# Performance work log

Measured on AMD Instinct MI355X. Metric: run time of the kernel, lower is better.

The kernel has to match this reference:

```python
import jax, jax.numpy as jnp
import numpy as np
from jax.scipy.special import i0

IM_SIZE = (256, 256)
GRID_SIZE = (512, 512)
NUMPOINTS = 6
OS = GRID_SIZE[0] / IM_SIZE[0]
# Beatty et al. optimal Kaiser-Bessel shape parameter
BETA = float(np.pi * np.sqrt((NUMPOINTS / OS) ** 2 * (OS - 0.5) ** 2 - 0.8))


def _apod_1d(N, G):
    # 1/FT(kb kernel) scaling coefficients (de-apodization), static numpy
    x = np.arange(N) - N / 2.0
    arg = np.pi * NUMPOINTS * x / G
    t = BETA ** 2 - arg ** 2  # > 0 for this config
    ph = np.sinh(np.sqrt(t)) / np.sqrt(t)
    return (1.0 / ph).astype(np.float32)


def _kb(u):
    # Kaiser-Bessel interpolation kernel, support |u| <= NUMPOINTS/2
    x = 2.0 * u / NUMPOINTS
    t = 1.0 - x * x
    inside = t > 0
    t = jnp.where(inside, t, 0.0)
    return jnp.where(inside, i0(BETA * jnp.sqrt(t)), 0.0)


def setup_inputs():
    key = jax.random.key(0)
    k1, k2, k3 = jax.random.split(key, 3)
    B, M = 8, 131072
    image = jax.random.normal(k1, (B,) + IM_SIZE, dtype=jnp.float32)
    ktraj = (jax.random.uniform(k2, (B, 2, M), dtype=jnp.float32) * 2.0 - 1.0) * jnp.pi
    dcf = jax.random.uniform(k3, (B, M), dtype=jnp.float32)
    return {"image": image, "ktraj": ktraj, "dcf": dcf}


def _nufft(image, ktraj, dcf):
    B = image.shape[0]
    N1, N2 = IM_SIZE
    G1, G2 = GRID_SIZE
    J = NUMPOINTS
    # 1) de-apodization (scaling coefficients), separable per-dim
    a1 = jnp.asarray(_apod_1d(N1, G1))
    a2 = jnp.asarray(_apod_1d(N2, G2))
    img = image.astype(jnp.complex64) * (a1[:, None] * a2[None, :])
    # 2) centered zero-pad to oversampled grid, FFT with DC at bin 0
    p1, p2 = (G1 - N1) // 2, (G2 - N2) // 2
    grid = jnp.zeros((B, G1, G2), dtype=jnp.complex64).at[:, p1:p1 + N1, p2:p2 + N2].set(img)
    kgrid = jnp.fft.fft2(jnp.fft.ifftshift(grid, axes=(1, 2)))
    # 3) KB interpolation (gather) at non-uniform points
    tm1 = ktraj[:, 0] * (G1 / (2.0 * jnp.pi))  # (B,M) in grid units
    tm2 = ktraj[:, 1] * (G2 / (2.0 * jnp.pi))
    offs = jnp.arange(J, dtype=jnp.float32) - (J // 2 - 1)  # [-2..3]
    g1 = jnp.floor(tm1)[..., None] + offs  # (B,M,J) neighbor coords
    g2 = jnp.floor(tm2)[..., None] + offs
    w1 = _kb(tm1[..., None] - g1)
    w2 = _kb(tm2[..., None] - g2)
    i1 = jnp.mod(g1.astype(jnp.int32), G1)
    i2 = jnp.mod(g2.astype(jnp.int32), G2)
    lin = (i1[..., :, None] * G2 + i2[..., None, :]).reshape(B, -1)  # (B, M*J*J)
    vals = jnp.take_along_axis(kgrid.reshape(B, -1), lin, axis=1).reshape(B, -1, J, J)
    w = (w1[..., :, None] * w2[..., None, :]).astype(jnp.complex64)
    kdata = jnp.sum(vals * w, axis=(-1, -2))  # (B,M) complex
    kdata = kdata * dcf
    return jnp.stack([kdata.real, kdata.imag], axis=0)  # (2,B,M) float32


def reference(image, ktraj, dcf):
    return _nufft(image, ktraj, dcf)
```

## Files before the change

kernel.cpp:

```cpp
#include <hip/hip_runtime.h>
#include <math.h>

#define GSZ 512
#define NSZ 256
#define NBATCH 8
#define MPTS 131072
#define PI_F 3.14159265358979f
#define BETA_F 13.8551004f
#define BETA2_F (BETA_F * BETA_F)
#define RSQ2 0.70710678f
#define PADIDX(i) ((i) + ((i) >> 3))

typedef float f32x4 __attribute__((ext_vector_type(4)));


__device__ __forceinline__ float apod(int i) {
    float x = (float)(i - 128);
    float arg = PI_F * 6.0f * x * (1.0f / 512.0f);
    float t = BETA2_F - arg * arg;
    float st = sqrtf(t);
    return 2.0f * st * __expf(-st);
}

__device__ __forceinline__ float kbw(float u) {
    float t = 1.0f - u * u * (1.0f / 9.0f);
    float x = BETA_F * sqrtf(fmaxf(t, 0.0f));
    float xc = fmaxf(x, 0.35f);
    float R = __builtin_amdgcn_rsqf(xc);
    float R2 = R * R;
    float q = R * (0.39894228f + R2 * (0.04986779f + R2 * 0.02804702f));
    float w = __expf(xc) * q;
    return (t > 0.0f) ? w : 0.0f;
}

template<int CTRL>
__device__ __forceinline__ float qdpp(float v) {
    int r = __builtin_amdgcn_mov_dpp(__float_as_int(v), CTRL, 0xF, 0xF, true);
    return __int_as_float(r);
}

__device__ __forceinline__ float2 cadd(float2 a, float2 b){ return make_float2(a.x+b.x, a.y+b.y); }
__device__ __forceinline__ float2 csub(float2 a, float2 b){ return make_float2(a.x-b.x, a.y-b.y); }
__device__ __forceinline__ float2 cmul(float2 a, float2 b){ return make_float2(a.x*b.x-a.y*b.y, a.x*b.y+a.y*b.x); }
__device__ __forceinline__ float2 mul_negi(float2 a){ return make_float2(a.y, -a.x); }
__device__ __forceinline__ float2 mul_posi(float2 a){ return make_float2(-a.y, a.x); }
__device__ __forceinline__ float2 mul_w81(float2 a){ return make_float2(RSQ2*(a.x+a.y), RSQ2*(a.y-a.x)); }
__device__ __forceinline__ float2 mul_w83(float2 a){ return make_float2(RSQ2*(a.y-a.x), -RSQ2*(a.x+a.y)); }

__device__ __forceinline__ void dft8_combine(float2 E0, float2 E1, float2 E2, float2 E3,
                                             float2 O0, float2 O1, float2 O2, float2 O3,
                                             float2* y) {
    float2 c1 = mul_w81(O1), c2 = mul_negi(O2), c3 = mul_w83(O3);
    y[0] = cadd(E0, O0); y[4] = csub(E0, O0);
    y[1] = cadd(E1, c1); y[5] = csub(E1, c1);
    y[2] = cadd(E2, c2); y[6] = csub(E2, c2);
    y[3] = cadd(E3, c3); y[7] = csub(E3, c3);
}

__device__ __forceinline__ void dft8(const float2* x, float2* y) {
    float2 a0=x[0], a1=x[2], a2=x[4], a3=x[6];
    float2 b0=x[1], b1=x[3], b2=x[5], b3=x[7];
    float2 ta0=cadd(a0,a2), ta1=csub(a0,a2), ta2=cadd(a1,a3), ta3=csub(a1,a3);
    float2 E0=cadd(ta0,ta2), E2=csub(ta0,ta2);
    float2 E1=cadd(ta1, mul_negi(ta3)), E3=cadd(ta1, mul_posi(ta3));
    float2 tb0=cadd(b0,b2), tb1=csub(b0,b2), tb2=cadd(b1,b3), tb3=csub(b1,b3);
    float2 O0=cadd(tb0,tb2), O2=csub(tb0,tb2);
    float2 O1=cadd(tb1, mul_negi(tb3)), O3=cadd(tb1, mul_posi(tb3));
    dft8_combine(E0,E1,E2,E3,O0,O1,O2,O3,y);
}

__device__ __forceinline__ void dft8_pruned(float2 x0, float2 x1, float2 x6, float2 x7, float2* y) {
    float2 E0 = cadd(x0, x6), E2 = csub(x0, x6);
    float2 E1 = cadd(x0, mul_posi(x6)), E3 = cadd(x0, mul_negi(x6));
    float2 O0 = cadd(x1, x7), O2 = csub(x1, x7);
    float2 O1 = cadd(x1, mul_posi(x7)), O3 = cadd(x1, mul_negi(x7));
    dft8_combine(E0,E1,E2,E3,O0,O1,O2,O3,y);
}

template<int S>
__device__ __forceinline__ void twiddle8(int t, float2* y) {
    if (S < 2) {
        int j = (S == 0) ? t : (t >> 3);
        const float scale = (S == 0) ? (-2.0f*PI_F/512.0f) : (-2.0f*PI_F/64.0f);
        float theta = scale * (float)j;
        float sn, cs;
        __sincosf(theta, &sn, &cs);
        float2 w = make_float2(cs, sn), wq = w;
        y[1] = cmul(y[1], wq);
        #pragma unroll
        for (int q = 2; q < 8; ++q) { wq = cmul(wq, w); y[q] = cmul(y[q], wq); }
    }
}


__device__ __forceinline__ float2 pswap(float2 v) {
    return make_float2(qdpp<0xB1>(v.x), qdpp<0xB1>(v.y));
}

__device__ __forceinline__ void dft8_half(const float2* v, float2* EO) {
    float2 t0 = cadd(v[0], v[2]), t1 = csub(v[0], v[2]);
    float2 t2 = cadd(v[1], v[3]), t3 = csub(v[1], v[3]);
    EO[0] = cadd(t0, t2); EO[2] = csub(t0, t2);
    EO[1] = cadd(t1, mul_negi(t3)); EO[3] = cadd(t1, mul_posi(t3));
}

__device__ __forceinline__ void dft8p_half(float2 u0, float2 u1, float2* EO) {
    EO[0] = cadd(u0, u1); EO[2] = csub(u0, u1);
    EO[1] = cadd(u0, mul_posi(u1)); EO[3] = cadd(u0, mul_negi(u1));
}

__device__ __forceinline__ void combine_half(int h, const float2* V, float2* y) {
    float2 P0 = pswap(V[0]), P1 = pswap(V[1]), P2 = pswap(V[2]), P3 = pswap(V[3]);
    float2 E0 = h ? P0 : V[0], O0 = h ? V[0] : P0;
    float2 E1 = h ? P1 : V[1], O1 = h ? V[1] : P1;
    float2 E2 = h ? P2 : V[2], O2 = h ? V[2] : P2;
    float2 E3 = h ? P3 : V[3], O3 = h ? V[3] : P3;
    float2 c1 = mul_w81(O1), c2 = mul_negi(O2), c3 = mul_w83(O3);
    float s = h ? -1.0f : 1.0f;
    y[0] = make_float2(fmaf(s, O0.x, E0.x), fmaf(s, O0.y, E0.y));
    y[1] = make_float2(fmaf(s, c1.x, E1.x), fmaf(s, c1.y, E1.y));
    y[2] = make_float2(fmaf(s, c2.x, E2.x), fmaf(s, c2.y, E2.y));
    y[3] = make_float2(fmaf(s, c3.x, E3.x), fmaf(s, c3.y, E3.y));
}

__device__ __forceinline__ void twiddle4h(int jidx, float scale, int h, float2* y) {
    float theta = scale * (float)jidx;
    float sn, cs;
    __sincosf(theta, &sn, &cs);
    float2 w = make_float2(cs, sn);
    float2 w2 = cmul(w, w);
    float2 w4 = cmul(w2, w2);
    float2 m = h ? w4 : make_float2(1.0f, 0.0f);
    y[0] = cmul(y[0], m);
    float2 wq = cmul(m, w); y[1] = cmul(y[1], wq);
    wq = cmul(wq, w);       y[2] = cmul(y[2], wq);
    wq = cmul(wq, w);       y[3] = cmul(y[3], wq);
}

__global__ __launch_bounds__(256) void pass1_rowfft(const float* __restrict__ image,
                                                    float2* __restrict__ T,
                                                    const float* __restrict__ ktraj,
                                                    const float* __restrict__ dcf,
                                                    int* __restrict__ cursors,
                                                    float4* __restrict__ sortedpt) {
    __shared__ float4 smemBuf[2176];
    int tid = threadIdx.x;
    int blk = blockIdx.x;

    if (blk >= 512) {
        int u = blk - 512;
        int bs = u >> 6, seg = u & 63;
        const float SCALE = (float)GSZ / (2.0f * PI_F);
        const float* kt1 = ktraj + (size_t)(bs * 2) * MPTS;
        const float* kt2 = kt1 + MPTS;
        const float* dcfb = dcf + ((size_t)bs << 17);
        int* cur = cursors + (bs << 7);
        float4* sp = sortedpt + ((size_t)bs << 18);

        float4* pts = smemBuf;
        int* hist = (int*)(smemBuf + 2048);
        int* lofs = hist + 128;
        int* gbase = hist + 256;
        int* lcur = hist + 384;

        if (tid < 128) hist[tid] = 0;
        __syncthreads();

        float t1v[8], t2v[8], dv[8];
        #pragma unroll
        for (int k = 0; k < 8; ++k) {
            int m = (seg << 11) + (k << 8) + tid;
            t1v[k] = kt1[m] * SCALE;
            t2v[k] = kt2[m] * SCALE;
            dv[k]  = dcfb[m];
            int key = (((int)floorf(t2v[k])) & 511) >> 2;
            atomicAdd(&hist[key], 1);
        }
        __syncthreads();

        if (tid == 0) {
            int s = 0;
            #pragma unroll 8
            for (int i = 0; i < 128; ++i) { lofs[i] = s; s += hist[i]; }
        }
        if (tid < 128) { gbase[tid] = atomicAdd(cur + tid, hist[tid]); lcur[tid] = 0; }
        __syncthreads();

        #pragma unroll
        for (int k = 0; k < 8; ++k) {
            int m = (seg << 11) + (k << 8) + tid;
            int key = (((int)floorf(t2v[k])) & 511) >> 2;
            int loc = atomicAdd(&lcur[key], 1);
            pts[lofs[key] + loc] =
                make_float4(t1v[k], t2v[k], dv[k], __int_as_float((key << 17) | m));
        }
        __syncthreads();

        #pragma unroll
        for (int k = 0; k < 8; ++k) {
            int s = (k << 8) + tid;
            float4 p = pts[s];
            int w = __float_as_int(p.w);
            int key = w >> 17;
            int m = w & 0x1FFFF;
            int gpos = gbase[key] + (s - lofs[key]);
            if (gpos < 2048)
                sp[((size_t)key << 11) + gpos] =
                    make_float4(p.x, p.y, p.z, __int_as_float(m));
        }
        return;
    }

    float2 (*sm)[2][578] = reinterpret_cast<float2(*)[2][578]>(smemBuf);
    int r = tid >> 7;
    int tt = tid & 127;
    int h = tt & 1;
    int b = tt >> 1;
    int p = blk & 3;
    int g = blk >> 2;
    int rp = (g << 1) + r;
    int y = (rp < 128) ? rp : (rp + 256);
    int iy = (y < 128) ? (y + 128) : (y - 384);
    float ay = apod(iy);
    const float* irow0 = image + ((size_t)((2 * p)     * NSZ + iy)) * NSZ;
    const float* irow1 = image + ((size_t)((2 * p + 1) * NSZ + iy)) * NSZ;

    float2 y4[4];
    {
        int iA = h ? (b + 192) : (b + 128);
        int iB = h ? (b + 64)  : b;
        float wA = ay * apod(iA), wB = ay * apod(iB);
        float2 u0 = make_float2(irow0[iA] * wA, irow1[iA] * wA);
        float2 u1 = make_float2(irow0[iB] * wB, irow1[iB] * wB);
        float2 EO[4];
        dft8p_half(u0, u1, EO);
        combine_half(h, EO, y4);
        twiddle4h(b, -2.0f * PI_F / 512.0f, h, y4);
    }
    float2* A  = sm[0][r];
    float2* Bf = sm[1][r];
    #pragma unroll
    for (int qq = 0; qq < 4; ++qq) A[PADIDX((b << 3) + (h << 2) + qq)] = y4[qq];
    __syncthreads();
    {
        float2 v[4];
        #pragma unroll
        for (int i = 0; i < 4; ++i) v[i] = A[PADIDX(b + (((i << 1) + h) << 6))];
        float2 EO[4];
        dft8_half(v, EO);
        combine_half(h, EO, y4);
        twiddle4h(b >> 3, -2.0f * PI_F / 64.0f, h, y4);
        int base = (b & 7) + ((b >> 3) << 6);
        #pragma unroll
        for (int qq = 0; qq < 4; ++qq) Bf[PADIDX(base + (((h << 2) + qq) << 3))] = y4[qq];
    }
    __syncthreads();
    {
        float2 v[4];
        #pragma unroll
        for (int i = 0; i < 4; ++i) v[i] = Bf[PADIDX(b + (((i << 1) + h) << 6))];
        float2 EO[4];
        dft8_half(v, EO);
        combine_half(h, EO, y4);
        float2* Trow = T + (((size_t)(p << 8) + rp) << 9);
        #pragma unroll
        for (int qq = 0; qq < 4; ++qq) Trow[b + (((h << 2) + qq) << 6)] = y4[qq];
    }
}

__global__ __launch_bounds__(256) void pass2_colfft(const float2* __restrict__ T,
                                                    float2* __restrict__ kgridT) {
    __shared__ float2 B[8][578];
    int tid = threadIdx.x;
    int blk = blockIdx.x;
    int p = blk & 3;
    int g = blk >> 2;
    const float2* Tb = T + ((size_t)p << 17);
    float2* Kb0 = kgridT + ((size_t)(2 * p) << 18);
    float2* Kb1 = Kb0 + ((size_t)1 << 18);

    #define COLG(c) ((g > 0) ? (((c) < 4) ? ((g << 2) + (c)) : (505 - (g << 2) + (c))) \
                             : (((c) < 4) ? (c) : (((c) == 7) ? 256 : (505 + (c)))))

    {
        int c = tid & 7, r0 = tid >> 3;
        int colg = COLG(c);
        #pragma unroll
        for (int k = 0; k < 8; ++k) {
            int rr = r0 + (k << 5);
            B[c][PADIDX(rr)] = Tb[((size_t)rr << 9) + colg];
        }
    }
    __syncthreads();
    int t = tid & 63;
    int c0 = tid >> 6;
    float2* Ba = B[c0];
    float2* Bb = B[c0 + 4];
    float2 ya[8], yb[8];
    {
        float2 a0 = Ba[PADIDX(t)],       a1 = Ba[PADIDX(t + 64)];
        float2 a6 = Ba[PADIDX(t + 128)], a7 = Ba[PADIDX(t + 192)];
        float2 b0 = Bb[PADIDX(t)],       b1 = Bb[PADIDX(t + 64)];
        float2 b6 = Bb[PADIDX(t + 128)], b7 = Bb[PADIDX(t + 192)];
        dft8_pruned(a0, a1, a6, a7, ya); twiddle8<0>(t, ya);
        dft8_pruned(b0, b1, b6, b7, yb); twiddle8<0>(t, yb);
    }
    __syncthreads();
    #pragma unroll
    for (int q = 0; q < 8; ++q) {
        Ba[PADIDX((t << 3) + q)] = ya[q];
        Bb[PADIDX((t << 3) + q)] = yb[q];
    }
    __syncthreads();
    {
        float2 xa[8], xb[8];
        #pragma unroll
        for (int pp = 0; pp < 8; ++pp) { xa[pp] = Ba[PADIDX(t + (pp << 6))]; xb[pp] = Bb[PADIDX(t + (pp << 6))]; }
        dft8(xa, ya); twiddle8<1>(t, ya);
        dft8(xb, yb); twiddle8<1>(t, yb);
    }
    __syncthreads();
    {
        int j = t >> 3, k = t & 7, base = k + (j << 6);
        #pragma unroll
        for (int q = 0; q < 8; ++q) {
            Ba[PADIDX(base + (q << 3))] = ya[q];
            Bb[PADIDX(base + (q << 3))] = yb[q];
        }
    }
    __syncthreads();
    {
        float2 xa[8], xb[8];
        #pragma unroll
        for (int pp = 0; pp < 8; ++pp) { xa[pp] = Ba[PADIDX(t + (pp << 6))]; xb[pp] = Bb[PADIDX(t + (pp << 6))]; }
        dft8(xa, ya);
        dft8(xb, yb);
    }
    __syncthreads();
    #pragma unroll
    for (int q = 0; q < 8; ++q) {
        Ba[PADIDX(t + (q << 6))] = ya[q];
        Bb[PADIDX(t + (q << 6))] = yb[q];
    }
    __syncthreads();
    {
        int c = tid & 7, r0 = tid >> 3;
        int colg = COLG(c);
        int mc = 7 - c;
        if (g == 0) { if (c == 0) mc = 0; else if (c == 7) mc = 7; }
        #pragma unroll
        for (int k = 0; k < 16; ++k) {
            int rr = r0 + (k << 5);
            int mr = (512 - rr) & 511;
            float2 Z = B[c][PADIDX(rr)];
            float2 M = B[mc][PADIDX(mr)];
            float2 K0 = make_float2(0.5f * (Z.x + M.x), 0.5f * (Z.y - M.y));
            float2 K1 = make_float2(0.5f * (Z.y + M.y), 0.5f * (M.x - Z.x));
            size_t off = ((size_t)colg << 9) + rr;
            Kb0[off] = K0;
            Kb1[off] = K1;
        }
    }
    #undef COLG
}

__global__ __launch_bounds__(256) void interp_kb(const float2* __restrict__ kgridT,
                                                 const int* __restrict__ cursors,
                                                 const float4* __restrict__ sortedpt,
                                                 float* __restrict__ out) {
    __shared__ float lds[9 * 1028];
    int tid = threadIdx.x;
    int blk = blockIdx.x;
    int b = blk & 7;
    int band = blk >> 3;
    int j = tid & 3;
    int q = tid >> 2;
    int j2 = j << 1;
    float fjm2 = (float)(j - 2), fjp2 = (float)(j + 2);

    int cnt = cursors[(b << 7) + band];
    cnt = (cnt > 2048) ? 2048 : cnt;
    if (cnt == 0) return;

    const float2* Kb = kgridT + ((size_t)b << 18);
    #pragma unroll
    for (int r = 0; r < 9; ++r) {
        int gc = ((band << 2) - 2 + r) & 511;
        const float4* src = (const float4*)(Kb + ((size_t)gc << 9));
        *(float4*)(lds + r * 1028 + (tid << 2)) = src[tid];
    }
    __syncthreads();

    const float4* sp = sortedpt + ((size_t)b << 18) + ((size_t)band << 11);
    float* out_re = out + ((size_t)b << 17);
    float* out_im = out_re + (size_t)NBATCH * MPTS;

    int iters = (cnt + 63) >> 6;
    for (int it = 0; it < iters; ++it) {
        int pidx = (it << 6) + q;
        bool valid = pidx < cnt;
        float4 pt = sp[valid ? pidx : 0];
        float tm1 = pt.x, tm2 = pt.y, dd = pt.z;
        int m = __float_as_int(pt.w);

        float f1 = floorf(tm1), f2 = floorf(tm2);
        int if1 = (int)f1, if2 = (int)f2;
        int e1 = (if1 - 2) & ~1;
        int rpair = (e1 + j2) & 511;
        int csoff = (if2 & 511) - (band << 2);

        float u1 = tm1 - (float)(e1 + j2);
        float wra = kbw(u1);
        float wrb = kbw(u1 - 1.0f);
        float fr2 = tm2 - f2;
        float wA = kbw(fr2 - fjm2);
        float wB = kbw(fr2 - fjp2);
        float w0_ = qdpp<0x00>(wA);
        float w1_ = qdpp<0x55>(wA);
        float w2_ = qdpp<0xAA>(wA);
        float w3_ = qdpp<0xFF>(wA);
        float w4_ = qdpp<0x00>(wB);
        float w5_ = qdpp<0x55>(wB);

        const float* lp = lds + (rpair << 1) + csoff * 1028;
        f32x4 v0 = *(const f32x4*)(lp + 0 * 1028);
        f32x4 v1 = *(const f32x4*)(lp + 1 * 1028);
        f32x4 v2 = *(const f32x4*)(lp + 2 * 1028);
        f32x4 v3 = *(const f32x4*)(lp + 3 * 1028);
        f32x4 v4 = *(const f32x4*)(lp + 4 * 1028);
        f32x4 v5 = *(const f32x4*)(lp + 5 * 1028);

        float c0re = w0_ * v0.x, c0im = w0_ * v0.y;
        float c1re = w0_ * v0.z, c1im = w0_ * v0.w;
        c0re = fmaf(w1_, v1.x, c0re); c0im = fmaf(w1_, v1.y, c0im);
        c1re = fmaf(w1_, v1.z, c1re); c1im = fmaf(w1_, v1.w, c1im);
        c0re = fmaf(w2_, v2.x, c0re); c0im = fmaf(w2_, v2.y, c0im);
        c1re = fmaf(w2_, v2.z, c1re); c1im = fmaf(w2_, v2.w, c1im);
        c0re = fmaf(w3_, v3.x, c0re); c0im = fmaf(w3_, v3.y, c0im);
        c1re = fmaf(w3_, v3.z, c1re); c1im = fmaf(w3_, v3.w, c1im);
        c0re = fmaf(w4_, v4.x, c0re); c0im = fmaf(w4_, v4.y, c0im);
        c1re = fmaf(w4_, v4.z, c1re); c1im = fmaf(w4_, v4.w, c1im);
        c0re = fmaf(w5_, v5.x, c0re); c0im = fmaf(w5_, v5.y, c0im);
        c1re = fmaf(w5_, v5.z, c1re); c1im = fmaf(w5_, v5.w, c1im);
        float p_re = fmaf(wra, c0re, wrb * c1re);
        float p_im = fmaf(wra, c0im, wrb * c1im);
        p_re += qdpp<0xB1>(p_re); p_re += qdpp<0x4E>(p_re);
        p_im += qdpp<0xB1>(p_im); p_im += qdpp<0x4E>(p_im);

        if (valid) {
            if (j == 0) out_re[m] = p_re * dd;
            else if (j == 1) out_im[m] = p_im * dd;
        }
    }
}


extern "C" void kernel_launch(void* const* d_in, const int* in_sizes, int n_in,
                              void* d_out, int out_size, void* d_ws, size_t ws_size,
                              hipStream_t stream) {
    const float* image = (const float*)d_in[0];
    const float* ktraj = (const float*)d_in[1];
    const float* dcf   = (const float*)d_in[2];
    float* out = (float*)d_out;

    float2* T        = (float2*)d_ws;
    float2* kgridT   = T + (size_t)4 * 256 * GSZ;
    int*    cursors  = (int*)((char*)d_ws + 20971520);
    float4* sortedpt = (float4*)((char*)d_ws + 20975616);

    hipMemsetAsync(cursors, 0, 1024 * sizeof(int), stream);
    pass1_rowfft<<<1024, 256, 0, stream>>>(image, T, ktraj, dcf, cursors, sortedpt);
    pass2_colfft<<<256, 256, 0, stream>>>(T, kgridT);
    interp_kb<<<1024, 256, 0, stream>>>(kgridT, cursors, sortedpt, out);
}
```

Baseline: 120.9 us.

## Split column FFT across 1024 threads with half-radix work and skip zero-weight LDS loads

The column FFT kernel now launches 1024 threads per block instead of 256. Each thread pair shares one radix-8 butterfly through the half-DFT and DPP combine helpers already used in the row pass, so each thread holds 4 values instead of 16. The old full dft8 helpers are deleted. In the interpolation kernel, the six LDS vector loads are now guarded so they are skipped when both row weights are zero. The changes aim to raise parallelism and cut register pressure in the column pass, at the cost of more threads per block and cross-lane shuffles. The guard adds a branch that may cause divergence.

```diff
diff --git a/kernel.cpp b/kernel.cpp
--- a/kernel.cpp
+++ b/kernel.cpp
@@ -46,51 +46,6 @@
 __device__ __forceinline__ float2 mul_posi(float2 a){ return make_float2(-a.y, a.x); }
 __device__ __forceinline__ float2 mul_w81(float2 a){ return make_float2(RSQ2*(a.x+a.y), RSQ2*(a.y-a.x)); }
 __device__ __forceinline__ float2 mul_w83(float2 a){ return make_float2(RSQ2*(a.y-a.x), -RSQ2*(a.x+a.y)); }
-
-__device__ __forceinline__ void dft8_combine(float2 E0, float2 E1, float2 E2, float2 E3,
-                                             float2 O0, float2 O1, float2 O2, float2 O3,
-                                             float2* y) {
-    float2 c1 = mul_w81(O1), c2 = mul_negi(O2), c3 = mul_w83(O3);
-    y[0] = cadd(E0, O0); y[4] = csub(E0, O0);
-    y[1] = cadd(E1, c1); y[5] = csub(E1, c1);
-    y[2] = cadd(E2, c2); y[6] = csub(E2, c2);
-    y[3] = cadd(E3, c3); y[7] = csub(E3, c3);
-}
-
-__device__ __forceinline__ void dft8(const float2* x, float2* y) {
-    float2 a0=x[0], a1=x[2], a2=x[4], a3=x[6];
-    float2 b0=x[1], b1=x[3], b2=x[5], b3=x[7];
-    float2 ta0=cadd(a0,a2), ta1=csub(a0,a2), ta2=cadd(a1,a3), ta3=csub(a1,a3);
-    float2 E0=cadd(ta0,ta2), E2=csub(ta0,ta2);
-    float2 E1=cadd(ta1, mul_negi(ta3)), E3=cadd(ta1, mul_posi(ta3));
-    float2 tb0=cadd(b0,b2), tb1=csub(b0,b2), tb2=cadd(b1,b3), tb3=csub(b1,b3);
-    float2 O0=cadd(tb0,tb2), O2=csub(tb0,tb2);
-    float2 O1=cadd(tb1, mul_negi(tb3)), O3=cadd(tb1, mul_posi(tb3));
-    dft8_combine(E0,E1,E2,E3,O0,O1,O2,O3,y);
-}
-
-__device__ __forceinline__ void dft8_pruned(float2 x0, float2 x1, float2 x6, float2 x7, float2* y) {
-    float2 E0 = cadd(x0, x6), E2 = csub(x0, x6);
-    float2 E1 = cadd(x0, mul_posi(x6)), E3 = cadd(x0, mul_negi(x6));
-    float2 O0 = cadd(x1, x7), O2 = csub(x1, x7);
-    float2 O1 = cadd(x1, mul_posi(x7)), O3 = cadd(x1, mul_negi(x7));
-    dft8_combine(E0,E1,E2,E3,O0,O1,O2,O3,y);
-}
-
-template<int S>
-__device__ __forceinline__ void twiddle8(int t, float2* y) {
-    if (S < 2) {
-        int j = (S == 0) ? t : (t >> 3);
-        const float scale = (S == 0) ? (-2.0f*PI_F/512.0f) : (-2.0f*PI_F/64.0f);
-        float theta = scale * (float)j;
-        float sn, cs;
-        __sincosf(theta, &sn, &cs);
-        float2 w = make_float2(cs, sn), wq = w;
-        y[1] = cmul(y[1], wq);
-        #pragma unroll
-        for (int q = 2; q < 8; ++q) { wq = cmul(wq, w); y[q] = cmul(y[q], wq); }
-    }
-}
 
 
 __device__ __forceinline__ float2 pswap(float2 v) {
@@ -268,8 +223,8 @@
     }
 }
 
-__global__ __launch_bounds__(256) void pass2_colfft(const float2* __restrict__ T,
-                                                    float2* __restrict__ kgridT) {
+__global__ __launch_bounds__(1024) void pass2_colfft(const float2* __restrict__ T,
+                                                     float2* __restrict__ kgridT) {
     __shared__ float2 B[8][578];
     int tid = threadIdx.x;
     int blk = blockIdx.x;
@@ -286,62 +241,59 @@
         int c = tid & 7, r0 = tid >> 3;
         int colg = COLG(c);
         #pragma unroll
-        for (int k = 0; k < 8; ++k) {
-            int rr = r0 + (k << 5);
+        for (int k = 0; k < 2; ++k) {
+            int rr = r0 + (k << 7);
             B[c][PADIDX(rr)] = Tb[((size_t)rr << 9) + colg];
         }
     }
     __syncthreads();
-    int t = tid & 63;
-    int c0 = tid >> 6;
-    float2* Ba = B[c0];
-    float2* Bb = B[c0 + 4];
-    float2 ya[8], yb[8];
-    {
-        float2 a0 = Ba[PADIDX(t)],       a1 = Ba[PADIDX(t + 64)];
-        float2 a6 = Ba[PADIDX(t + 128)], a7 = Ba[PADIDX(t + 192)];
-        float2 b0 = Bb[PADIDX(t)],       b1 = Bb[PADIDX(t + 64)];
-        float2 b6 = Bb[PADIDX(t + 128)], b7 = Bb[PADIDX(t + 192)];
-        dft8_pruned(a0, a1, a6, a7, ya); twiddle8<0>(t, ya);
-        dft8_pruned(b0, b1, b6, b7, yb); twiddle8<0>(t, yb);
+
+    int s = tid >> 7;
+    int tt = tid & 127;
+    int h = tt & 1;
+    int b = tt >> 1;
+    float2* Bs = B[s];
+    float2 y4[4];
+
+    {
+        float2 u0 = Bs[PADIDX(b + (h << 6))];
+        float2 u1 = Bs[PADIDX(b + 128 + (h << 6))];
+        float2 EO[4];
+        dft8p_half(u0, u1, EO);
+        combine_half(h, EO, y4);
+        twiddle4h(b, -2.0f * PI_F / 512.0f, h, y4);
     }
     __syncthreads();
     #pragma unroll
-    for (int q = 0; q < 8; ++q) {
-        Ba[PADIDX((t << 3) + q)] = ya[q];
-        Bb[PADIDX((t << 3) + q)] = yb[q];
-    }
-    __syncthreads();
-    {
-        float2 xa[8], xb[8];
-        #pragma unroll
-        for (int pp = 0; pp < 8; ++pp) { xa[pp] = Ba[PADIDX(t + (pp << 6))]; xb[pp] = Bb[PADIDX(t + (pp << 6))]; }
-        dft8(xa, ya); twiddle8<1>(t, ya);
-        dft8(xb, yb); twiddle8<1>(t, yb);
-    }
-    __syncthreads();
-    {
-        int j = t >> 3, k = t & 7, base = k + (j << 6);
-        #pragma unroll
-        for (int q = 0; q < 8; ++q) {
-            Ba[PADIDX(base + (q << 3))] = ya[q];
-            Bb[PADIDX(base + (q << 3))] = yb[q];
-        }
-    }
-    __syncthreads();
-    {
-        float2 xa[8], xb[8];
-        #pragma unroll
-        for (int pp = 0; pp < 8; ++pp) { xa[pp] = Ba[PADIDX(t + (pp << 6))]; xb[pp] = Bb[PADIDX(t + (pp << 6))]; }
-        dft8(xa, ya);
-        dft8(xb, yb);
+    for (int qq = 0; qq < 4; ++qq) Bs[PADIDX((b << 3) + (h << 2) + qq)] = y4[qq];
+    __syncthreads();
+    {
+        float2 v[4];
+        #pragma unroll
+        for (int i = 0; i < 4; ++i) v[i] = Bs[PADIDX(b + (((i << 1) + h) << 6))];
+        float2 EO[4];
+        dft8_half(v, EO);
+        combine_half(h, EO, y4);
+        twiddle4h(b >> 3, -2.0f * PI_F / 64.0f, h, y4);
+    }
+    __syncthreads();
+    {
+        int base = (b & 7) + ((b >> 3) << 6);
+        #pragma unroll
+        for (int qq = 0; qq < 4; ++qq) Bs[PADIDX(base + (((h << 2) + qq) << 3))] = y4[qq];
+    }
+    __syncthreads();
+    {
+        float2 v[4];
+        #pragma unroll
+        for (int i = 0; i < 4; ++i) v[i] = Bs[PADIDX(b + (((i << 1) + h) << 6))];
+        float2 EO[4];
+        dft8_half(v, EO);
+        combine_half(h, EO, y4);
     }
     __syncthreads();
     #pragma unroll
-    for (int q = 0; q < 8; ++q) {
-        Ba[PADIDX(t + (q << 6))] = ya[q];
-        Bb[PADIDX(t + (q << 6))] = yb[q];
-    }
+    for (int qq = 0; qq < 4; ++qq) Bs[PADIDX(b + (((h << 2) + qq) << 6))] = y4[qq];
     __syncthreads();
     {
         int c = tid & 7, r0 = tid >> 3;
@@ -349,8 +301,8 @@
         int mc = 7 - c;
         if (g == 0) { if (c == 0) mc = 0; else if (c == 7) mc = 7; }
         #pragma unroll
-        for (int k = 0; k < 16; ++k) {
-            int rr = r0 + (k << 5);
+        for (int k = 0; k < 4; ++k) {
+            int rr = r0 + (k << 7);
             int mr = (512 - rr) & 511;
             float2 Z = B[c][PADIDX(rr)];
             float2 M = B[mc][PADIDX(mr)];
@@ -422,13 +374,17 @@
         float w4_ = qdpp<0x00>(wB);
         float w5_ = qdpp<0x55>(wB);
 
-        const float* lp = lds + (rpair << 1) + csoff * 1028;
-        f32x4 v0 = *(const f32x4*)(lp + 0 * 1028);
-        f32x4 v1 = *(const f32x4*)(lp + 1 * 1028);
-        f32x4 v2 = *(const f32x4*)(lp + 2 * 1028);
-        f32x4 v3 = *(const f32x4*)(lp + 3 * 1028);
-        f32x4 v4 = *(const f32x4*)(lp + 4 * 1028);
-        f32x4 v5 = *(const f32x4*)(lp + 5 * 1028);
+        f32x4 v0 = {0,0,0,0}, v1 = {0,0,0,0}, v2 = {0,0,0,0};
+        f32x4 v3 = {0,0,0,0}, v4 = {0,0,0,0}, v5 = {0,0,0,0};
+        if (wra != 0.0f || wrb != 0.0f) {
+            const float* lp = lds + (rpair << 1) + csoff * 1028;
+            v0 = *(const f32x4*)(lp + 0 * 1028);
+            v1 = *(const f32x4*)(lp + 1 * 1028);
+            v2 = *(const f32x4*)(lp + 2 * 1028);
+            v3 = *(const f32x4*)(lp + 3 * 1028);
+            v4 = *(const f32x4*)(lp + 4 * 1028);
+            v5 = *(const f32x4*)(lp + 5 * 1028);
+        }
 
         float c0re = w0_ * v0.x, c0im = w0_ * v0.y;
         float c1re = w0_ * v0.z, c1im = w0_ * v0.w;
@@ -470,6 +426,6 @@
 
     hipMemsetAsync(cursors, 0, 1024 * sizeof(int), stream);
     pass1_rowfft<<<1024, 256, 0, stream>>>(image, T, ktraj, dcf, cursors, sortedpt);
-    pass2_colfft<<<256, 256, 0, stream>>>(T, kgridT);
+    pass2_colfft<<<256, 1024, 0, stream>>>(T, kgridT);
     interp_kb<<<1024, 256, 0, stream>>>(kgridT, cursors, sortedpt, out);
 }
```

Result: slower. 123.5 us (+2.1%).
